# Performance work log

Measured on AMD Instinct MI355X. Metric: run time of the kernel, lower is better.

Reference implementation:

```python
import jax, jax.numpy as jnp
import numpy as np

N = 50000
E = 800000
D_IN = 256
D_HID = 256
D_OUT = 256
EPS = 1e-5


def _sage_conv(x, src, dst, Wl, Wr, b, n_nodes):
    # mean aggregation of source-node features at target nodes (PyG SAGEConv default)
    msg = x[src]                                              # [E, d_in]
    agg = jax.ops.segment_sum(msg, dst, num_segments=n_nodes)  # [N, d_in]
    deg = jax.ops.segment_sum(jnp.ones((src.shape[0],), x.dtype), dst,
                              num_segments=n_nodes)           # [N]
    agg = agg / jnp.maximum(deg, 1.0)[:, None]
    return agg @ Wl + x @ Wr + b


def _bn(h, gamma, beta, mean, var):
    # inference-mode BatchNorm1d
    return (h - mean) * jax.lax.rsqrt(var + EPS) * gamma + beta


def setup_inputs() -> dict:
    key = jax.random.key(0)
    ks = jax.random.split(key, 16)
    x = jax.random.normal(ks[0], (N, D_IN), dtype=jnp.float32)
    edge_index = jax.random.randint(ks[1], (2, E), 0, N, dtype=jnp.int32)

    def lin(k, din, dout):
        return jax.random.normal(k, (din, dout), dtype=jnp.float32) / np.sqrt(din)

    inp = {"x": x, "edge_index": edge_index}
    dims = [(D_IN, D_HID), (D_HID, D_HID), (D_HID, D_OUT)]
    ki = 2
    for i, (din, dout) in enumerate(dims):
        inp[f"Wl{i}"] = lin(ks[ki], din, dout); ki += 1
        inp[f"Wr{i}"] = lin(ks[ki], din, dout); ki += 1
        inp[f"b{i}"] = jnp.zeros((dout,), jnp.float32)
    for i in range(2):
        inp[f"gamma{i}"] = jnp.ones((D_HID,), jnp.float32)
        inp[f"beta{i}"] = jnp.zeros((D_HID,), jnp.float32)
        inp[f"mean{i}"] = jax.random.normal(ks[ki], (D_HID,), jnp.float32) * 0.1; ki += 1
        inp[f"var{i}"] = jnp.ones((D_HID,), jnp.float32) + 0.1 * jax.random.uniform(ks[ki], (D_HID,)); ki += 1
    return inp


def reference(x, edge_index, Wl0, Wr0, b0, Wl1, Wr1, b1, Wl2, Wr2, b2,
              gamma0, beta0, mean0, var0, gamma1, beta1, mean1, var1):
    src, dst = edge_index[0], edge_index[1]
    h = x
    layers = [(Wl0, Wr0, b0, gamma0, beta0, mean0, var0),
              (Wl1, Wr1, b1, gamma1, beta1, mean1, var1)]
    for Wl, Wr, b, g, bt, m, v in layers:
        h_res = h
        h = _sage_conv(h, src, dst, Wl, Wr, b, N)
        h = jax.nn.relu(_bn(h, g, bt, m, v))
        # dropout is identity in eval mode
        if h_res.shape[1] == h.shape[1]:
            h = h + h_res
    return _sage_conv(h, src, dst, Wl2, Wr2, b2, N)
```

## Files before the change

### kernel.cpp

```cpp
#include <hip/hip_runtime.h>
#include <hip/hip_bf16.h>

#define NN 50000
#define NE 800000
#define DD 256
#define EPSV 1e-5f

typedef float f32x4 __attribute__((ext_vector_type(4)));
typedef short bf16x8s __attribute__((ext_vector_type(8)));

__device__ __forceinline__ float bf2f(unsigned short u) {
  unsigned int x = ((unsigned int)u) << 16;
  return __builtin_bit_cast(float, x);
}
__device__ __forceinline__ unsigned short f2bf(float f) {
  return __builtin_bit_cast(unsigned short, __float2bfloat16(f));
}

__device__ __forceinline__ void mfma_bf16(bf16x8s a, bf16x8s b, f32x4& c) {
  asm("v_mfma_f32_16x16x32_bf16 %0, %1, %2, %0" : "+v"(c) : "v"(a), "v"(b));
}

__device__ __forceinline__ void gload_lds16(const void* g, void* l) {
  __builtin_amdgcn_global_load_lds((const __attribute__((address_space(1))) void*)g,
                                   (__attribute__((address_space(3))) void*)l, 16, 0, 0);
}


__global__ void deg_count_k(const int* __restrict__ ei, int* __restrict__ deg) {
  int e = blockIdx.x * 256 + threadIdx.x;
  if (e < NE) atomicAdd(&deg[ei[NE + e]], 1);
}

__global__ void scan1_k(const int* __restrict__ deg, int* __restrict__ row_ptr,
                        int* __restrict__ blockSums) {
  __shared__ int s[1024];
  int gid = blockIdx.x * 1024 + threadIdx.x;
  int v = (gid < NN) ? deg[gid] : 0;
  s[threadIdx.x] = v;
  __syncthreads();
  for (int off = 1; off < 1024; off <<= 1) {
    int t = (threadIdx.x >= off) ? s[threadIdx.x - off] : 0;
    __syncthreads();
    s[threadIdx.x] += t;
    __syncthreads();
  }
  if (gid < NN) row_ptr[gid] = s[threadIdx.x] - v;
  if (threadIdx.x == 1023) blockSums[blockIdx.x] = s[1023];
}

__global__ void scan2_k(const int* __restrict__ blockSums, int* __restrict__ blockOffs,
                        int* __restrict__ row_ptr, int nblocks) {
  if (threadIdx.x == 0) {
    int run = 0;
    for (int i = 0; i < nblocks; ++i) { blockOffs[i] = run; run += blockSums[i]; }
    row_ptr[NN] = run;
  }
}

__global__ void scan3_k(int* __restrict__ row_ptr, const int* __restrict__ blockOffs,
                        const int* __restrict__ deg, float* __restrict__ deg_inv) {
  int gid = blockIdx.x * 1024 + threadIdx.x;
  if (gid < NN) {
    row_ptr[gid] += blockOffs[blockIdx.x];
    deg_inv[gid] = 1.0f / (float)max(deg[gid], 1);
  }
}

__global__ void csr_fill_k(const int* __restrict__ ei, int* __restrict__ cursor,
                           int* __restrict__ col_idx) {
  int e = blockIdx.x * 256 + threadIdx.x;
  if (e < NE) {
    int pos = atomicAdd(&cursor[ei[NE + e]], 1);
    col_idx[pos] = ei[e];
  }
}


__global__ __launch_bounds__(256) void split_x_k(const float* __restrict__ x,
                                                 unsigned short* __restrict__ xhi,
                                                 unsigned short* __restrict__ xlo) {
  int gid = blockIdx.x * 256 + threadIdx.x;
  float4 v = reinterpret_cast<const float4*>(x)[gid];
  float f[4] = {v.x, v.y, v.z, v.w};
  ushort4 hi, lo;
  unsigned short* hp = &hi.x; unsigned short* lp = &lo.x;
#pragma unroll
  for (int c = 0; c < 4; ++c) {
    unsigned short h = f2bf(f[c]);
    hp[c] = h;
    lp[c] = f2bf(f[c] - bf2f(h));
  }
  reinterpret_cast<ushort4*>(xhi)[gid] = hi;
  reinterpret_cast<ushort4*>(xlo)[gid] = lo;
}


__global__ __launch_bounds__(256) void wtprep_k(const float* __restrict__ W,
                                                unsigned short* __restrict__ thi,
                                                unsigned short* __restrict__ tlo) {
  int gid = blockIdx.x * 256 + threadIdx.x;
  int n = gid >> 6, k4 = (gid & 63) << 2;
  ushort4 hi, lo;
  unsigned short* hp = &hi.x; unsigned short* lp = &lo.x;
#pragma unroll
  for (int r = 0; r < 4; ++r) {
    float v = W[(size_t)(k4 + r) * DD + n];
    unsigned short h = f2bf(v);
    hp[r] = h;
    lp[r] = f2bf(v - bf2f(h));
  }
  *reinterpret_cast<ushort4*>(thi + (size_t)n * DD + k4) = hi;
  *reinterpret_cast<ushort4*>(tlo + (size_t)n * DD + k4) = lo;
}


__global__ __launch_bounds__(256) void sage_agg_k(
    const unsigned short* __restrict__ hhi, const unsigned short* __restrict__ hlo,
    const int* __restrict__ row_ptr, const int* __restrict__ col_idx,
    const float* __restrict__ deg_inv,
    unsigned short* __restrict__ ahi, unsigned short* __restrict__ alo) {
  int wave = threadIdx.x >> 6;
  int lane = threadIdx.x & 63;
  int node = blockIdx.x * 4 + wave;
  int beg = row_ptr[node], end = row_ptr[node + 1];
  float a0 = 0.f, a1 = 0.f, a2 = 0.f, a3 = 0.f;
  for (int e = beg; e < end; ++e) {
    int s = col_idx[e];
    ushort4 vh = *(reinterpret_cast<const ushort4*>(hhi + (size_t)s * DD) + lane);
    ushort4 vl = *(reinterpret_cast<const ushort4*>(hlo + (size_t)s * DD) + lane);
    a0 += bf2f(vh.x) + bf2f(vl.x);
    a1 += bf2f(vh.y) + bf2f(vl.y);
    a2 += bf2f(vh.z) + bf2f(vl.z);
    a3 += bf2f(vh.w) + bf2f(vl.w);
  }
  float di = deg_inv[node];
  float f[4] = {a0 * di, a1 * di, a2 * di, a3 * di};
  ushort4 hi, lo;
  unsigned short* hp = &hi.x; unsigned short* lp = &lo.x;
#pragma unroll
  for (int c = 0; c < 4; ++c) {
    unsigned short h = f2bf(f[c]);
    hp[c] = h;
    lp[c] = f2bf(f[c] - bf2f(h));
  }
  *(reinterpret_cast<ushort4*>(ahi + (size_t)node * DD) + lane) = hi;
  *(reinterpret_cast<ushort4*>(alo + (size_t)node * DD) + lane) = lo;
}


template <bool DO_BN>
__global__ __launch_bounds__(256) void sage_gemm_k(
    const unsigned short* __restrict__ aHi, const unsigned short* __restrict__ aLo,
    const unsigned short* __restrict__ hHi, const unsigned short* __restrict__ hLo,
    const unsigned short* __restrict__ wlHi, const unsigned short* __restrict__ wlLo,
    const unsigned short* __restrict__ wrHi, const unsigned short* __restrict__ wrLo,
    const float* __restrict__ bias,
    const float* __restrict__ gamma, const float* __restrict__ beta,
    const float* __restrict__ mean, const float* __restrict__ var,
    float* __restrict__ outF, unsigned short* __restrict__ outHi,
    unsigned short* __restrict__ outLo) {
  __shared__ __attribute__((aligned(128))) char lds[32768];
  const int AHI = 0, ALO = 8192, BHI = 16384, BLO = 24576;

  int tid = threadIdx.x, wave = tid >> 6, lane = tid & 63;
  int wr = wave >> 1, wc = wave & 1;
  int m0 = blockIdx.x * 128, n0 = blockIdx.y * 128;
  int lr = lane & 15, lq = lane >> 4;

  f32x4 acc[4][4];
#pragma unroll
  for (int i = 0; i < 4; ++i)
#pragma unroll
    for (int j = 0; j < 4; ++j) acc[i][j] = (f32x4)0.f;

  for (int kt = 0; kt < 16; ++kt) {
    int kbase = kt * 32;
    bool first = kbase < 256;
    const unsigned short* Ah_ = first ? aHi : hHi;
    const unsigned short* Al_ = first ? aLo : hLo;
    const unsigned short* Bh_ = first ? wlHi : wrHi;
    const unsigned short* Bl_ = first ? wlLo : wrLo;
    int kh = (kbase & 255) + lq * 8;

#pragma unroll
    for (int t = 0; t < 2; ++t) {
      int mi = wave * 2 + t;
      int gm = m0 + mi * 16 + lr;
      gm = gm < NN ? gm : NN - 1;
      gload_lds16(Ah_ + (size_t)gm * DD + kh, &lds[AHI + mi * 1024]);
      gload_lds16(Al_ + (size_t)gm * DD + kh, &lds[ALO + mi * 1024]);
      int gn = n0 + mi * 16 + lr;
      gload_lds16(Bh_ + (size_t)gn * DD + kh, &lds[BHI + mi * 1024]);
      gload_lds16(Bl_ + (size_t)gn * DD + kh, &lds[BLO + mi * 1024]);
    }
    __syncthreads();

    bf16x8s fbhi[4], fblo[4];
#pragma unroll
    for (int j = 0; j < 4; ++j) {
      int offb = (wc * 4 + j) * 1024 + lane * 16;
      fbhi[j] = *reinterpret_cast<const bf16x8s*>(&lds[BHI + offb]);
      fblo[j] = *reinterpret_cast<const bf16x8s*>(&lds[BLO + offb]);
    }
#pragma unroll
    for (int i = 0; i < 4; ++i) {
      int offa = (wr * 4 + i) * 1024 + lane * 16;
      bf16x8s fahi = *reinterpret_cast<const bf16x8s*>(&lds[AHI + offa]);
      bf16x8s falo = *reinterpret_cast<const bf16x8s*>(&lds[ALO + offa]);
#pragma unroll
      for (int j = 0; j < 4; ++j) {
        mfma_bf16(fahi, fbhi[j], acc[i][j]);
        mfma_bf16(fahi, fblo[j], acc[i][j]);
        mfma_bf16(falo, fbhi[j], acc[i][j]);
      }
    }
    __syncthreads();
  }

#pragma unroll
  for (int j = 0; j < 4; ++j) {
    int n = n0 + wc * 64 + j * 16 + lr;
    float bb = bias[n], sc = 0.f, sh = 0.f;
    if (DO_BN) {
      float s = gamma[n] * rsqrtf(var[n] + EPSV);
      sc = s;
      sh = beta[n] - mean[n] * s;
    }
#pragma unroll
    for (int i = 0; i < 4; ++i) {
#pragma unroll
      for (int r = 0; r < 4; ++r) {
        int m = m0 + wr * 64 + i * 16 + lq * 4 + r;
        if (m < NN) {
          float v = acc[i][j][r] + bb;
          size_t idx = (size_t)m * DD + n;
          if (DO_BN) {
            v = fmaxf(v * sc + sh, 0.f);
            v += bf2f(hHi[idx]) + bf2f(hLo[idx]);
            unsigned short h = f2bf(v);
            outHi[idx] = h;
            outLo[idx] = f2bf(v - bf2f(h));
          } else {
            outF[idx] = v;
          }
        }
      }
    }
  }
}


extern "C" void kernel_launch(void* const* d_in, const int* in_sizes, int n_in,
                              void* d_out, int out_size, void* d_ws, size_t ws_size,
                              hipStream_t stream) {
  const float* x   = (const float*)d_in[0];
  const int*   ei  = (const int*)d_in[1];
  const float* Wl[3] = {(const float*)d_in[2], (const float*)d_in[5], (const float*)d_in[8]};
  const float* Wr[3] = {(const float*)d_in[3], (const float*)d_in[6], (const float*)d_in[9]};
  const float* bs[3] = {(const float*)d_in[4], (const float*)d_in[7], (const float*)d_in[10]};
  const float* g0  = (const float*)d_in[11];
  const float* be0 = (const float*)d_in[12];
  const float* mu0 = (const float*)d_in[13];
  const float* va0 = (const float*)d_in[14];
  const float* g1  = (const float*)d_in[15];
  const float* be1 = (const float*)d_in[16];
  const float* mu1 = (const float*)d_in[17];
  const float* va1 = (const float*)d_in[18];
  float* out = (float*)d_out;

  char* w = (char*)d_ws;
  const size_t o_deg    = 0;
  const size_t o_rowptr = 262144;
  const size_t o_cursor = 524288;
  const size_t o_colidx = 786432;
  const size_t o_deginv = 4194304;
  const size_t o_bsum   = 4456448;
  const size_t o_boff   = 4460544;
  const size_t o_wt     = 4464640;
  const size_t PLANE    = (size_t)NN * DD * 2;
  const size_t o_xhi    = 6291456;
  const size_t o_xlo    = o_xhi + PLANE;
  const size_t o_h1hi   = o_xhi + 2 * PLANE;
  const size_t o_h1lo   = o_xhi + 3 * PLANE;
  const size_t o_agghi  = o_xhi + 4 * PLANE;
  const size_t o_agglo  = o_xhi + 5 * PLANE;

  int*   deg     = (int*)(w + o_deg);
  int*   row_ptr = (int*)(w + o_rowptr);
  int*   cursor  = (int*)(w + o_cursor);
  int*   col_idx = (int*)(w + o_colidx);
  float* deg_inv = (float*)(w + o_deginv);
  int*   bsum    = (int*)(w + o_bsum);
  int*   boff    = (int*)(w + o_boff);
  unsigned short* wt    = (unsigned short*)(w + o_wt);
  unsigned short* xhi   = (unsigned short*)(w + o_xhi);
  unsigned short* xlo   = (unsigned short*)(w + o_xlo);
  unsigned short* h1hi  = (unsigned short*)(w + o_h1hi);
  unsigned short* h1lo  = (unsigned short*)(w + o_h1lo);
  unsigned short* agghi = (unsigned short*)(w + o_agghi);
  unsigned short* agglo = (unsigned short*)(w + o_agglo);

  unsigned short* wlT[3][2];
  unsigned short* wrT[3][2];
  for (int l = 0; l < 3; ++l) {
    wlT[l][0] = wt + (size_t)(4 * l + 0) * 65536;
    wlT[l][1] = wt + (size_t)(4 * l + 1) * 65536;
    wrT[l][0] = wt + (size_t)(4 * l + 2) * 65536;
    wrT[l][1] = wt + (size_t)(4 * l + 3) * 65536;
  }

  const int SCAN_BLOCKS = (NN + 1023) / 1024;

  hipMemsetAsync(deg, 0, NN * sizeof(int), stream);
  deg_count_k<<<NE / 256, 256, 0, stream>>>(ei, deg);
  scan1_k<<<SCAN_BLOCKS, 1024, 0, stream>>>(deg, row_ptr, bsum);
  scan2_k<<<1, 64, 0, stream>>>(bsum, boff, row_ptr, SCAN_BLOCKS);
  scan3_k<<<SCAN_BLOCKS, 1024, 0, stream>>>(row_ptr, boff, deg, deg_inv);
  hipMemcpyAsync(cursor, row_ptr, NN * sizeof(int), hipMemcpyDeviceToDevice, stream);
  csr_fill_k<<<NE / 256, 256, 0, stream>>>(ei, cursor, col_idx);

  split_x_k<<<NN * DD / 4 / 256, 256, 0, stream>>>(x, xhi, xlo);
  for (int l = 0; l < 3; ++l) {
    wtprep_k<<<64, 256, 0, stream>>>(Wl[l], wlT[l][0], wlT[l][1]);
    wtprep_k<<<64, 256, 0, stream>>>(Wr[l], wrT[l][0], wrT[l][1]);
  }

  dim3 ggrid((NN + 127) / 128, 2);

  sage_agg_k<<<NN / 4, 256, 0, stream>>>(xhi, xlo, row_ptr, col_idx, deg_inv, agghi, agglo);
  sage_gemm_k<true><<<ggrid, 256, 0, stream>>>(agghi, agglo, xhi, xlo,
                                               wlT[0][0], wlT[0][1], wrT[0][0], wrT[0][1],
                                               bs[0], g0, be0, mu0, va0,
                                               nullptr, h1hi, h1lo);
  sage_agg_k<<<NN / 4, 256, 0, stream>>>(h1hi, h1lo, row_ptr, col_idx, deg_inv, agghi, agglo);
  sage_gemm_k<true><<<ggrid, 256, 0, stream>>>(agghi, agglo, h1hi, h1lo,
                                               wlT[1][0], wlT[1][1], wrT[1][0], wrT[1][1],
                                               bs[1], g1, be1, mu1, va1,
                                               nullptr, xhi, xlo);
  sage_agg_k<<<NN / 4, 256, 0, stream>>>(xhi, xlo, row_ptr, col_idx, deg_inv, agghi, agglo);
  sage_gemm_k<false><<<ggrid, 256, 0, stream>>>(agghi, agglo, xhi, xlo,
                                                wlT[2][0], wlT[2][1], wrT[2][0], wrT[2][1],
                                                bs[2], nullptr, nullptr, nullptr, nullptr,
                                                out, nullptr, nullptr);
}
```

Before: 926.7 us.

## Interleave hi/lo bf16 activations in column-chunked layout and double-buffer GEMM

Activations are now stored as 16 column chunks per node, each chunk holding 16 hi and 16 lo bf16 values together, instead of separate hi and lo planes. Aggregation is split across 16 chunk blocks so a gather touches contiguous 64-byte pieces, with edges unrolled by four. The GEMM switches to 64-row tiles spanning all 256 output columns with a double-buffered LDS pipeline, so the A tile is loaded only once per block. Weight prep is merged into a single launch. The chunked layout can mean more scattered small gathers and more GEMM blocks, and the 80 KB of LDS per block may limit occupancy.

```diff
diff --git a/kernel.cpp b/kernel.cpp
--- a/kernel.cpp
+++ b/kernel.cpp
@@ -8,9 +8,10 @@
 
 typedef float f32x4 __attribute__((ext_vector_type(4)));
 typedef short bf16x8s __attribute__((ext_vector_type(8)));
-
-__device__ __forceinline__ float bf2f(unsigned short u) {
-  unsigned int x = ((unsigned int)u) << 16;
+typedef unsigned int uint32;
+
+__device__ __forceinline__ float bf2f(unsigned int u16) {
+  unsigned int x = u16 << 16;
   return __builtin_bit_cast(float, x);
 }
 __device__ __forceinline__ unsigned short f2bf(float f) {
@@ -25,6 +26,7 @@
   __builtin_amdgcn_global_load_lds((const __attribute__((address_space(1))) void*)g,
                                    (__attribute__((address_space(3))) void*)l, 16, 0, 0);
 }
+
 
 
 __global__ void deg_count_k(const int* __restrict__ ei, int* __restrict__ deg) {
@@ -78,27 +80,43 @@
 
 
 __global__ __launch_bounds__(256) void split_x_k(const float* __restrict__ x,
-                                                 unsigned short* __restrict__ xhi,
-                                                 unsigned short* __restrict__ xlo) {
-  int gid = blockIdx.x * 256 + threadIdx.x;
-  float4 v = reinterpret_cast<const float4*>(x)[gid];
-  float f[4] = {v.x, v.y, v.z, v.w};
-  ushort4 hi, lo;
-  unsigned short* hp = &hi.x; unsigned short* lp = &lo.x;
-#pragma unroll
-  for (int c = 0; c < 4; ++c) {
-    unsigned short h = f2bf(f[c]);
-    hp[c] = h;
-    lp[c] = f2bf(f[c] - bf2f(h));
-  }
-  reinterpret_cast<ushort4*>(xhi)[gid] = hi;
-  reinterpret_cast<ushort4*>(xlo)[gid] = lo;
-}
-
-
-__global__ __launch_bounds__(256) void wtprep_k(const float* __restrict__ W,
-                                                unsigned short* __restrict__ thi,
-                                                unsigned short* __restrict__ tlo) {
+                                                 uint32* __restrict__ xc) {
+  int ni = threadIdx.x & 15, c = threadIdx.x >> 4;
+  int node = blockIdx.x * 16 + ni;
+  const float4* xr = reinterpret_cast<const float4*>(x + (size_t)node * DD + c * 16);
+  float f[16];
+#pragma unroll
+  for (int q = 0; q < 4; ++q) {
+    float4 v = xr[q];
+    f[q * 4 + 0] = v.x; f[q * 4 + 1] = v.y; f[q * 4 + 2] = v.z; f[q * 4 + 3] = v.w;
+  }
+  uint32 wbuf[16];
+#pragma unroll
+  for (int g = 0; g < 8; ++g) {
+    unsigned short h0 = f2bf(f[2 * g]), h1 = f2bf(f[2 * g + 1]);
+    unsigned short l0 = f2bf(f[2 * g] - bf2f(h0));
+    unsigned short l1 = f2bf(f[2 * g + 1] - bf2f(h1));
+    wbuf[g] = (uint32)h0 | ((uint32)h1 << 16);
+    wbuf[8 + g] = (uint32)l0 | ((uint32)l1 << 16);
+  }
+  uint32* dst = xc + ((size_t)c * NN + node) * 16;
+#pragma unroll
+  for (int q = 0; q < 4; ++q)
+    reinterpret_cast<uint4*>(dst)[q] =
+        make_uint4(wbuf[q * 4], wbuf[q * 4 + 1], wbuf[q * 4 + 2], wbuf[q * 4 + 3]);
+}
+
+
+__global__ __launch_bounds__(256) void wtprep_k(
+    const float* __restrict__ W0, const float* __restrict__ W1,
+    const float* __restrict__ W2, const float* __restrict__ W3,
+    const float* __restrict__ W4, const float* __restrict__ W5,
+    unsigned short* __restrict__ wt) {
+  int p = blockIdx.y;
+  const float* W = (p == 0) ? W0 : (p == 1) ? W1 : (p == 2) ? W2
+                   : (p == 3) ? W3 : (p == 4) ? W4 : W5;
+  unsigned short* thi = wt + (size_t)(2 * p) * 65536;
+  unsigned short* tlo = wt + (size_t)(2 * p + 1) * 65536;
   int gid = blockIdx.x * 256 + threadIdx.x;
   int n = gid >> 6, k4 = (gid & 63) << 2;
   ushort4 hi, lo;
@@ -116,57 +134,61 @@
 
 
 __global__ __launch_bounds__(256) void sage_agg_k(
-    const unsigned short* __restrict__ hhi, const unsigned short* __restrict__ hlo,
-    const int* __restrict__ row_ptr, const int* __restrict__ col_idx,
-    const float* __restrict__ deg_inv,
-    unsigned short* __restrict__ ahi, unsigned short* __restrict__ alo) {
-  int wave = threadIdx.x >> 6;
-  int lane = threadIdx.x & 63;
-  int node = blockIdx.x * 4 + wave;
-  int beg = row_ptr[node], end = row_ptr[node + 1];
-  float a0 = 0.f, a1 = 0.f, a2 = 0.f, a3 = 0.f;
-  for (int e = beg; e < end; ++e) {
-    int s = col_idx[e];
-    ushort4 vh = *(reinterpret_cast<const ushort4*>(hhi + (size_t)s * DD) + lane);
-    ushort4 vl = *(reinterpret_cast<const ushort4*>(hlo + (size_t)s * DD) + lane);
-    a0 += bf2f(vh.x) + bf2f(vl.x);
-    a1 += bf2f(vh.y) + bf2f(vl.y);
-    a2 += bf2f(vh.z) + bf2f(vl.z);
-    a3 += bf2f(vh.w) + bf2f(vl.w);
-  }
+    const uint32* __restrict__ act, const int* __restrict__ rp,
+    const int* __restrict__ ci, const float* __restrict__ deg_inv,
+    uint32* __restrict__ agg) {
+  int c = blockIdx.y;
+  int node = blockIdx.x * 16 + (threadIdx.x >> 4);
+  int gl = threadIdx.x & 15;
+  const uint32* base = act + (size_t)c * NN * 16;
+  int beg = rp[node], end = rp[node + 1];
+  float s0 = 0.f, s1 = 0.f;
+  int e = beg;
+  for (; e + 4 <= end; e += 4) {
+    int n0 = ci[e], n1 = ci[e + 1], n2 = ci[e + 2], n3 = ci[e + 3];
+    uint32 u0 = base[(size_t)n0 * 16 + gl];
+    uint32 u1 = base[(size_t)n1 * 16 + gl];
+    uint32 u2 = base[(size_t)n2 * 16 + gl];
+    uint32 u3 = base[(size_t)n3 * 16 + gl];
+    s0 += (bf2f(u0 & 0xffff) + bf2f(u1 & 0xffff)) + (bf2f(u2 & 0xffff) + bf2f(u3 & 0xffff));
+    s1 += (bf2f(u0 >> 16) + bf2f(u1 >> 16)) + (bf2f(u2 >> 16) + bf2f(u3 >> 16));
+  }
+  for (; e < end; ++e) {
+    uint32 u = base[(size_t)ci[e] * 16 + gl];
+    s0 += bf2f(u & 0xffff);
+    s1 += bf2f(u >> 16);
+  }
+  float t0 = s0 + __shfl_xor(s0, 8);
+  float t1 = s1 + __shfl_xor(s1, 8);
   float di = deg_inv[node];
-  float f[4] = {a0 * di, a1 * di, a2 * di, a3 * di};
-  ushort4 hi, lo;
-  unsigned short* hp = &hi.x; unsigned short* lp = &lo.x;
-#pragma unroll
-  for (int c = 0; c < 4; ++c) {
-    unsigned short h = f2bf(f[c]);
-    hp[c] = h;
-    lp[c] = f2bf(f[c] - bf2f(h));
-  }
-  *(reinterpret_cast<ushort4*>(ahi + (size_t)node * DD) + lane) = hi;
-  *(reinterpret_cast<ushort4*>(alo + (size_t)node * DD) + lane) = lo;
+  t0 *= di; t1 *= di;
+  unsigned short h0 = f2bf(t0), h1 = f2bf(t1);
+  uint32 word;
+  if (gl < 8) {
+    word = (uint32)h0 | ((uint32)h1 << 16);
+  } else {
+    unsigned short l0 = f2bf(t0 - bf2f(h0));
+    unsigned short l1 = f2bf(t1 - bf2f(h1));
+    word = (uint32)l0 | ((uint32)l1 << 16);
+  }
+  agg[(size_t)c * NN * 16 + (size_t)node * 16 + gl] = word;
 }
 
 
 template <bool DO_BN>
 __global__ __launch_bounds__(256) void sage_gemm_k(
-    const unsigned short* __restrict__ aHi, const unsigned short* __restrict__ aLo,
-    const unsigned short* __restrict__ hHi, const unsigned short* __restrict__ hLo,
+    const unsigned short* __restrict__ aggC, const unsigned short* __restrict__ hC,
     const unsigned short* __restrict__ wlHi, const unsigned short* __restrict__ wlLo,
     const unsigned short* __restrict__ wrHi, const unsigned short* __restrict__ wrLo,
     const float* __restrict__ bias,
     const float* __restrict__ gamma, const float* __restrict__ beta,
     const float* __restrict__ mean, const float* __restrict__ var,
-    float* __restrict__ outF, unsigned short* __restrict__ outHi,
-    unsigned short* __restrict__ outLo) {
-  __shared__ __attribute__((aligned(128))) char lds[32768];
-  const int AHI = 0, ALO = 8192, BHI = 16384, BLO = 24576;
+    float* __restrict__ outF, unsigned short* __restrict__ outC) {
+  __shared__ __attribute__((aligned(128))) char lds[2][40960];
 
   int tid = threadIdx.x, wave = tid >> 6, lane = tid & 63;
-  int wr = wave >> 1, wc = wave & 1;
-  int m0 = blockIdx.x * 128, n0 = blockIdx.y * 128;
   int lr = lane & 15, lq = lane >> 4;
+  int m0 = blockIdx.x * 64;
 
   f32x4 acc[4][4];
 #pragma unroll
@@ -174,40 +196,44 @@
 #pragma unroll
     for (int j = 0; j < 4; ++j) acc[i][j] = (f32x4)0.f;
 
-  for (int kt = 0; kt < 16; ++kt) {
-    int kbase = kt * 32;
-    bool first = kbase < 256;
-    const unsigned short* Ah_ = first ? aHi : hHi;
-    const unsigned short* Al_ = first ? aLo : hLo;
-    const unsigned short* Bh_ = first ? wlHi : wrHi;
-    const unsigned short* Bl_ = first ? wlLo : wrLo;
-    int kh = (kbase & 255) + lq * 8;
-
-#pragma unroll
-    for (int t = 0; t < 2; ++t) {
-      int mi = wave * 2 + t;
-      int gm = m0 + mi * 16 + lr;
-      gm = gm < NN ? gm : NN - 1;
-      gload_lds16(Ah_ + (size_t)gm * DD + kh, &lds[AHI + mi * 1024]);
-      gload_lds16(Al_ + (size_t)gm * DD + kh, &lds[ALO + mi * 1024]);
-      int gn = n0 + mi * 16 + lr;
-      gload_lds16(Bh_ + (size_t)gn * DD + kh, &lds[BHI + mi * 1024]);
-      gload_lds16(Bl_ + (size_t)gn * DD + kh, &lds[BLO + mi * 1024]);
-    }
-    __syncthreads();
-
+  auto STAGE = [&](char* L, int kt) {
+    const unsigned short* act;
+    const unsigned short* wh;
+    const unsigned short* wl_;
+    if (kt < 8) { act = aggC; wh = wlHi; wl_ = wlLo; }
+    else        { act = hC;   wh = wrHi; wl_ = wrLo; }
+    int kk = (kt & 7) * 32 + lq * 8;
+    int cch = kk >> 4, ko = kk & 15;
+#pragma unroll
+    for (int t = 0; t < 10; ++t) {
+      int u = wave * 10 + t;
+      if (u < 8) {
+        int mi = u >> 1, pl = u & 1;
+        int gm = m0 + mi * 16 + lr;
+        gm = gm < NN ? gm : NN - 1;
+        gload_lds16(act + (size_t)(cch * NN + gm) * 32 + pl * 16 + ko,
+                    L + u * 1024 + lane * 16);
+      } else {
+        int v = u - 8, ni = v >> 1, pl = v & 1;
+        const unsigned short* w = pl ? wl_ : wh;
+        gload_lds16(w + (size_t)(ni * 16 + lr) * DD + kk,
+                    L + 8192 + v * 1024 + lane * 16);
+      }
+    }
+  };
+
+  auto COMPUTE = [&](const char* L) {
     bf16x8s fbhi[4], fblo[4];
 #pragma unroll
     for (int j = 0; j < 4; ++j) {
-      int offb = (wc * 4 + j) * 1024 + lane * 16;
-      fbhi[j] = *reinterpret_cast<const bf16x8s*>(&lds[BHI + offb]);
-      fblo[j] = *reinterpret_cast<const bf16x8s*>(&lds[BLO + offb]);
+      int ni = wave * 4 + j;
+      fbhi[j] = *reinterpret_cast<const bf16x8s*>(L + 8192 + ni * 2048 + lane * 16);
+      fblo[j] = *reinterpret_cast<const bf16x8s*>(L + 8192 + ni * 2048 + 1024 + lane * 16);
     }
 #pragma unroll
     for (int i = 0; i < 4; ++i) {
-      int offa = (wr * 4 + i) * 1024 + lane * 16;
-      bf16x8s fahi = *reinterpret_cast<const bf16x8s*>(&lds[AHI + offa]);
-      bf16x8s falo = *reinterpret_cast<const bf16x8s*>(&lds[ALO + offa]);
+      bf16x8s fahi = *reinterpret_cast<const bf16x8s*>(L + i * 2048 + lane * 16);
+      bf16x8s falo = *reinterpret_cast<const bf16x8s*>(L + i * 2048 + 1024 + lane * 16);
 #pragma unroll
       for (int j = 0; j < 4; ++j) {
         mfma_bf16(fahi, fbhi[j], acc[i][j]);
@@ -215,34 +241,46 @@
         mfma_bf16(falo, fbhi[j], acc[i][j]);
       }
     }
+  };
+
+  STAGE(lds[0], 0);
+  __syncthreads();
+  int cur = 0;
+#pragma unroll 1
+  for (int kt = 0; kt < 15; ++kt) {
+    STAGE(lds[cur ^ 1], kt + 1);
+    COMPUTE(lds[cur]);
     __syncthreads();
-  }
+    cur ^= 1;
+  }
+  COMPUTE(lds[cur]);
 
 #pragma unroll
   for (int j = 0; j < 4; ++j) {
-    int n = n0 + wc * 64 + j * 16 + lr;
+    int n = wave * 64 + j * 16 + lr;
     float bb = bias[n], sc = 0.f, sh = 0.f;
     if (DO_BN) {
       float s = gamma[n] * rsqrtf(var[n] + EPSV);
       sc = s;
       sh = beta[n] - mean[n] * s;
     }
+    int cch = n >> 4, o = n & 15;
 #pragma unroll
     for (int i = 0; i < 4; ++i) {
 #pragma unroll
       for (int r = 0; r < 4; ++r) {
-        int m = m0 + wr * 64 + i * 16 + lq * 4 + r;
+        int m = m0 + i * 16 + lq * 4 + r;
         if (m < NN) {
           float v = acc[i][j][r] + bb;
-          size_t idx = (size_t)m * DD + n;
           if (DO_BN) {
             v = fmaxf(v * sc + sh, 0.f);
-            v += bf2f(hHi[idx]) + bf2f(hLo[idx]);
+            size_t ub = (size_t)(cch * NN + m) * 32;
+            v += bf2f(hC[ub + o]) + bf2f(hC[ub + 16 + o]);
             unsigned short h = f2bf(v);
-            outHi[idx] = h;
-            outLo[idx] = f2bf(v - bf2f(h));
+            outC[ub + o] = h;
+            outC[ub + 16 + o] = f2bf(v - bf2f(h));
           } else {
-            outF[idx] = v;
+            outF[(size_t)m * DD + n] = v;
           }
         }
       }
@@ -278,13 +316,10 @@
   const size_t o_bsum   = 4456448;
   const size_t o_boff   = 4460544;
   const size_t o_wt     = 4464640;
-  const size_t PLANE    = (size_t)NN * DD * 2;
-  const size_t o_xhi    = 6291456;
-  const size_t o_xlo    = o_xhi + PLANE;
-  const size_t o_h1hi   = o_xhi + 2 * PLANE;
-  const size_t o_h1lo   = o_xhi + 3 * PLANE;
-  const size_t o_agghi  = o_xhi + 4 * PLANE;
-  const size_t o_agglo  = o_xhi + 5 * PLANE;
+  const size_t ACT      = (size_t)16 * NN * 64;
+  const size_t o_xC     = 6291456;
+  const size_t o_h1C    = o_xC + ACT;
+  const size_t o_aggC   = o_xC + 2 * ACT;
 
   int*   deg     = (int*)(w + o_deg);
   int*   row_ptr = (int*)(w + o_rowptr);
@@ -293,13 +328,10 @@
   float* deg_inv = (float*)(w + o_deginv);
   int*   bsum    = (int*)(w + o_bsum);
   int*   boff    = (int*)(w + o_boff);
-  unsigned short* wt    = (unsigned short*)(w + o_wt);
-  unsigned short* xhi   = (unsigned short*)(w + o_xhi);
-  unsigned short* xlo   = (unsigned short*)(w + o_xlo);
-  unsigned short* h1hi  = (unsigned short*)(w + o_h1hi);
-  unsigned short* h1lo  = (unsigned short*)(w + o_h1lo);
-  unsigned short* agghi = (unsigned short*)(w + o_agghi);
-  unsigned short* agglo = (unsigned short*)(w + o_agglo);
+  unsigned short* wt   = (unsigned short*)(w + o_wt);
+  uint32* xC   = (uint32*)(w + o_xC);
+  uint32* h1C  = (uint32*)(w + o_h1C);
+  uint32* aggC = (uint32*)(w + o_aggC);
 
   unsigned short* wlT[3][2];
   unsigned short* wrT[3][2];
@@ -320,27 +352,25 @@
   hipMemcpyAsync(cursor, row_ptr, NN * sizeof(int), hipMemcpyDeviceToDevice, stream);
   csr_fill_k<<<NE / 256, 256, 0, stream>>>(ei, cursor, col_idx);
 
-  split_x_k<<<NN * DD / 4 / 256, 256, 0, stream>>>(x, xhi, xlo);
-  for (int l = 0; l < 3; ++l) {
-    wtprep_k<<<64, 256, 0, stream>>>(Wl[l], wlT[l][0], wlT[l][1]);
-    wtprep_k<<<64, 256, 0, stream>>>(Wr[l], wrT[l][0], wrT[l][1]);
-  }
-
-  dim3 ggrid((NN + 127) / 128, 2);
-
-  sage_agg_k<<<NN / 4, 256, 0, stream>>>(xhi, xlo, row_ptr, col_idx, deg_inv, agghi, agglo);
-  sage_gemm_k<true><<<ggrid, 256, 0, stream>>>(agghi, agglo, xhi, xlo,
-                                               wlT[0][0], wlT[0][1], wrT[0][0], wrT[0][1],
-                                               bs[0], g0, be0, mu0, va0,
-                                               nullptr, h1hi, h1lo);
-  sage_agg_k<<<NN / 4, 256, 0, stream>>>(h1hi, h1lo, row_ptr, col_idx, deg_inv, agghi, agglo);
-  sage_gemm_k<true><<<ggrid, 256, 0, stream>>>(agghi, agglo, h1hi, h1lo,
-                                               wlT[1][0], wlT[1][1], wrT[1][0], wrT[1][1],
-                                               bs[1], g1, be1, mu1, va1,
-                                               nullptr, xhi, xlo);
-  sage_agg_k<<<NN / 4, 256, 0, stream>>>(xhi, xlo, row_ptr, col_idx, deg_inv, agghi, agglo);
-  sage_gemm_k<false><<<ggrid, 256, 0, stream>>>(agghi, agglo, xhi, xlo,
-                                                wlT[2][0], wlT[2][1], wrT[2][0], wrT[2][1],
-                                                bs[2], nullptr, nullptr, nullptr, nullptr,
-                                                out, nullptr, nullptr);
-}
+  split_x_k<<<NN / 16, 256, 0, stream>>>(x, xC);
+  wtprep_k<<<dim3(64, 6), 256, 0, stream>>>(Wl[0], Wr[0], Wl[1], Wr[1], Wl[2], Wr[2], wt);
+
+  dim3 agrid(NN / 16, 16);
+  dim3 ggrid((NN + 63) / 64);
+
+  sage_agg_k<<<agrid, 256, 0, stream>>>(xC, row_ptr, col_idx, deg_inv, aggC);
+  sage_gemm_k<true><<<ggrid, 256, 0, stream>>>(
+      (const unsigned short*)aggC, (const unsigned short*)xC,
+      wlT[0][0], wlT[0][1], wrT[0][0], wrT[0][1],
+      bs[0], g0, be0, mu0, va0, nullptr, (unsigned short*)h1C);
+  sage_agg_k<<<agrid, 256, 0, stream>>>(h1C, row_ptr, col_idx, deg_inv, aggC);
+  sage_gemm_k<true><<<ggrid, 256, 0, stream>>>(
+      (const unsigned short*)aggC, (const unsigned short*)h1C,
+      wlT[1][0], wlT[1][1], wrT[1][0], wrT[1][1],
+      bs[1], g1, be1, mu1, va1, nullptr, (unsigned short*)xC);
+  sage_agg_k<<<agrid, 256, 0, stream>>>(xC, row_ptr, col_idx, deg_inv, aggC);
+  sage_gemm_k<false><<<ggrid, 256, 0, stream>>>(
+      (const unsigned short*)aggC, (const unsigned short*)xC,
+      wlT[2][0], wlT[2][1], wrT[2][0], wrT[2][1],
+      bs[2], nullptr, nullptr, nullptr, nullptr, out, nullptr);
+}
```

Measured after the change: 1.002 ms. +8.2%, slower.
